# Optimization experiments

Hardware: AMD Instinct MI355X
Metric: run time of the kernel (lower is better)

Reference implementation:

```python
import jax, jax.numpy as jnp
import numpy as np
from jax import lax

T, D = 1024, 2048          # tokens, hidden
E, I = 32, 1408            # routed experts, expert intermediate
K = 6                      # top_k
N_GROUP, TOPK_GROUP = 8, 3
ROUTED_SCALE = 2.5
SHARED_I = 2 * I           # n_shared_experts * moe_intermediate_size


def setup_inputs() -> dict:
    key = jax.random.key(0)
    ks = jax.random.split(key, 9)
    s = lambda k, shape, fan: jax.random.normal(k, shape, jnp.float32) * (fan ** -0.5)
    return {
        "hidden_states": jax.random.normal(ks[0], (T, D), jnp.float32),
        "gate_w": s(ks[1], (D, E), D),
        "e_score_correction_bias": jax.random.normal(ks[2], (E,), jnp.float32) * 0.1,
        "w_gate": s(ks[3], (E, D, I), D),
        "w_up": s(ks[4], (E, D, I), D),
        "w_down": s(ks[5], (E, I, D), I),
        "ws_gate": s(ks[6], (D, SHARED_I), D),
        "ws_up": s(ks[7], (D, SHARED_I), D),
        "ws_down": s(ks[8], (SHARED_I, D), SHARED_I),
    }


def _route(x, gate_w, bias):
    """DeepSeek noaux_tc grouped top-k with sigmoid scoring."""
    logits = x @ gate_w                       # [T, E]
    scores = jax.nn.sigmoid(logits)
    scores_corr = scores + bias[None, :]
    # group scores = sum of top-2 corrected scores within each group
    g = scores_corr.reshape(-1, N_GROUP, E // N_GROUP)
    group_scores = lax.top_k(g, 2)[0].sum(-1)            # [T, n_group]
    _, gidx = lax.top_k(group_scores, TOPK_GROUP)        # [T, topk_group]
    gmask = jax.nn.one_hot(gidx, N_GROUP, dtype=scores.dtype).sum(1)  # [T, n_group]
    emask = jnp.repeat(gmask, E // N_GROUP, axis=-1)     # [T, E]
    masked = jnp.where(emask > 0, scores_corr, -jnp.inf)
    _, topk_idx = lax.top_k(masked, K)                   # [T, K]
    w = jnp.take_along_axis(scores, topk_idx, axis=-1)   # weights from UNcorrected scores
    w = w / (w.sum(-1, keepdims=True) + 1e-20)           # norm_topk_prob=True
    return topk_idx, w


def reference(hidden_states, gate_w, e_score_correction_bias,
              w_gate, w_up, w_down, ws_gate, ws_up, ws_down):
    x = hidden_states                                    # [T, D]
    topk_idx, topk_w = _route(x, gate_w, e_score_correction_bias)

    # combine weights as a sparse [T, E] matrix (K nonzeros per row)
    tok = jnp.arange(x.shape[0])[:, None]
    combine = jnp.zeros((x.shape[0], E), x.dtype).at[tok, topk_idx].add(topk_w)

    # routed experts: SwiGLU FFN per expert (dense-dispatch reference)
    h = jax.nn.silu(jnp.einsum('td,edi->eti', x, w_gate))
    h = h * jnp.einsum('td,edi->eti', x, w_up)           # [E, T, I]
    y = jnp.einsum('eti,eid->etd', h, w_down)            # [E, T, D]
    routed = jnp.einsum('te,etd->td', combine, y) * ROUTED_SCALE

    # shared experts MLP (SiluAndMul)
    shared = (jax.nn.silu(x @ ws_gate) * (x @ ws_up)) @ ws_down
    return routed + shared
```

## Files before the change

### kernel.cpp

```cpp
#include <hip/hip_runtime.h>

#define T_TOK 1024
#define D_HID 2048
#define NEXP 32
#define I_EXP 1408
#define TOPK 6
#define NGRP 8
#define GSIZE 4
#define TOPG 3
#define SHI 2816
#define RSCALE 2.5f

typedef __attribute__((ext_vector_type(8))) short short8;
typedef __attribute__((ext_vector_type(4))) float floatx4;

__device__ __forceinline__ unsigned short f2b(float f) {
  unsigned int u = __float_as_uint(f);
  u += 0x7fffu + ((u >> 16) & 1u);
  return (unsigned short)(u >> 16);
}

__device__ __forceinline__ void gld_lds16(const void* g, void* l) {
  __builtin_amdgcn_global_load_lds(
      (const __attribute__((address_space(1))) unsigned int*)g,
      (__attribute__((address_space(3))) unsigned int*)l, 16, 0, 0);
}

__device__ __forceinline__ uint4 pack8(const float* v) {
  uint4 o;
  o.x = (unsigned)f2b(v[0]) | ((unsigned)f2b(v[1]) << 16);
  o.y = (unsigned)f2b(v[2]) | ((unsigned)f2b(v[3]) << 16);
  o.z = (unsigned)f2b(v[4]) | ((unsigned)f2b(v[5]) << 16);
  o.w = (unsigned)f2b(v[6]) | ((unsigned)f2b(v[7]) << 16);
  return o;
}

__device__ __forceinline__ uint2 pack4(const float* v) {
  uint2 o;
  o.x = (unsigned)f2b(v[0]) | ((unsigned)f2b(v[1]) << 16);
  o.y = (unsigned)f2b(v[2]) | ((unsigned)f2b(v[3]) << 16);
  return o;
}

__global__ __launch_bounds__(64) void k_route(
    const float* __restrict__ x, const float* __restrict__ gw,
    const float* __restrict__ bias, int* __restrict__ tki, float* __restrict__ tkw)
{
  int t = blockIdx.x;
  __shared__ float xs[D_HID];
  __shared__ float sc[NEXP], cor[NEXP];
  int lane = threadIdx.x;
  for (int d = lane * 4; d < D_HID; d += 64 * 4)
    *(float4*)(xs + d) = *(const float4*)(x + (size_t)t * D_HID + d);
  __syncthreads();
  if (lane < NEXP) {
    float acc = 0.f;
    for (int d = 0; d < D_HID; ++d) acc += xs[d] * gw[d * NEXP + lane];
    float s = 1.f / (1.f + expf(-acc));
    sc[lane] = s;
    cor[lane] = s + bias[lane];
  }
  __syncthreads();
  if (lane == 0) {
    float gs[NGRP];
    for (int g = 0; g < NGRP; ++g) {
      float m1 = -INFINITY, m2 = -INFINITY;
      for (int j = 0; j < GSIZE; ++j) {
        float v = cor[g * GSIZE + j];
        if (v > m1) { m2 = m1; m1 = v; } else if (v > m2) m2 = v;
      }
      gs[g] = m1 + m2;
    }
    unsigned gmask = 0;
    for (int rr = 0; rr < TOPG; ++rr) {
      int bi = -1; float bv = -INFINITY;
      for (int g = 0; g < NGRP; ++g)
        if (!((gmask >> g) & 1) && gs[g] > bv) { bv = gs[g]; bi = g; }
      gmask |= 1u << bi;
    }
    unsigned used = 0;
    float wsum = 0.f;
    int idxs[TOPK]; float wsel[TOPK];
    for (int rr = 0; rr < TOPK; ++rr) {
      int bi = -1; float bv = -INFINITY;
      for (int e = 0; e < NEXP; ++e) {
        if (!((gmask >> (e / GSIZE)) & 1)) continue;
        if ((used >> e) & 1) continue;
        if (cor[e] > bv) { bv = cor[e]; bi = e; }
      }
      used |= 1u << bi;
      idxs[rr] = bi; wsel[rr] = sc[bi]; wsum += sc[bi];
    }
    float inv = 1.f / (wsum + 1e-20f);
    for (int rr = 0; rr < TOPK; ++rr) {
      tki[t * TOPK + rr] = idxs[rr];
      tkw[t * TOPK + rr] = wsel[rr] * inv;
    }
  }
}

__global__ __launch_bounds__(256) void k_count(const int* __restrict__ tki,
                                               int* __restrict__ cnt, int* __restrict__ offp)
{
  __shared__ int c[NEXP];
  if (threadIdx.x < NEXP) c[threadIdx.x] = 0;
  __syncthreads();
  for (int i = threadIdx.x; i < T_TOK * TOPK; i += 256) atomicAdd(&c[tki[i]], 1);
  __syncthreads();
  if (threadIdx.x == 0) {
    int s = 0;
    for (int e = 0; e < NEXP; ++e) { offp[e] = s; cnt[e] = c[e]; s += c[e]; }
    offp[NEXP] = s;
  }
}

__global__ __launch_bounds__(64) void k_compact(
    const int* __restrict__ tki, const float* __restrict__ tkw,
    const int* __restrict__ offp, int* __restrict__ tok, float* __restrict__ wts)
{
  int e = blockIdx.x, lane = threadIdx.x;
  int base = offp[e];
  for (int t0 = 0; t0 < T_TOK; t0 += 64) {
    int t = t0 + lane;
    int found = -1;
    for (int j = 0; j < TOPK; ++j)
      if (tki[t * TOPK + j] == e) found = j;
    unsigned long long m = __ballot(found >= 0);
    if (found >= 0) {
      int pos = base + __popcll(m & ((1ull << lane) - 1ull));
      tok[pos] = t;
      wts[pos] = tkw[t * TOPK + found];
    }
    base += __popcll(m);
  }
}

__global__ __launch_bounds__(256) void k_cast(const float* __restrict__ x,
                                              unsigned short* __restrict__ xb, int n4)
{
  int i = blockIdx.x * 256 + threadIdx.x;
  if (i < n4) {
    float4 v = ((const float4*)x)[i];
    ushort4 o;
    o.x = f2b(v.x); o.y = f2b(v.y); o.z = f2b(v.z); o.w = f2b(v.w);
    ((ushort4*)xb)[i] = o;
  }
}


template<int N, int K>
__device__ __forceinline__ void gemm_gu(
    const unsigned short* __restrict__ xb,
    const float* __restrict__ wgp, const float* __restrict__ wup,
    const int* __restrict__ tok, int rowbase, int nrows,
    unsigned short* __restrict__ hout, int n0,
    unsigned short* As , unsigned short* Bls )
{
  const int tid = threadIdx.x;
  const int wid = tid >> 6, lane = tid & 63;
  const int c = lane & 15, r = lane >> 4;
  const int wr = wid >> 1, wc = wid & 1;

  const int mat = wid >> 2;
  const int bko = wid & 3;
  const float* bsrc = (mat ? wup : wgp) + (size_t)(bko * 8) * N + n0 + lane;
  const int bwoff = lane * 36 + bko * 8 + mat * 2304;

  int aoff[4];
  #pragma unroll
  for (int mf = 0; mf < 4; ++mf)
    aoff[mf] = (r * 256 + wr * 64 + mf * 16 + c) * 8;
  int boff[2];
  #pragma unroll
  for (int nf = 0; nf < 2; ++nf)
    boff[nf] = (wc * 32 + nf * 16 + c) * 36 + r * 8;

  constexpr int NK = K / 32;

  for (int m0 = 0; m0 < nrows; m0 += 256) {
    const unsigned short* ga;
    {
      int rl = min(m0 + (tid & 255), nrows - 1);
      int tA = tok ? tok[rowbase + rl] : (rowbase + rl);
      ga = xb + (size_t)tA * K + (tid >> 8) * 8;
    }

    floatx4 accg[4][2] = {};
    floatx4 accu[4][2] = {};
    float br[8];

    #pragma unroll
    for (int j = 0; j < 8; ++j) br[j] = bsrc[(size_t)j * N];
    { uint4 pw = pack8(br); *(uint4*)&Bls[bwoff] = pw; }
    gld_lds16(ga, As + (size_t)tid * 8);
    gld_lds16(ga + 16, As + (size_t)(512 + tid) * 8);
    #pragma unroll
    for (int j = 0; j < 8; ++j) br[j] = bsrc[(size_t)(32 + j) * N];
    __syncthreads();

    int b = 0;
    for (int kt = 0; kt < NK; ++kt) {
      if (kt + 1 < NK) {
        { uint4 pw = pack8(br); *(uint4*)&Bls[(b ^ 1) * 4608 + bwoff] = pw; }
        const unsigned short* gap = ga + (kt + 1) * 32;
        gld_lds16(gap, As + (size_t)((b ^ 1) * 8192 + tid * 8));
        gld_lds16(gap + 16, As + (size_t)((b ^ 1) * 8192 + 4096 + tid * 8));
      }
      if (kt + 2 < NK) {
        const float* bs = bsrc + (size_t)(kt + 2) * 32 * N;
        #pragma unroll
        for (int j = 0; j < 8; ++j) br[j] = bs[(size_t)j * N];
      }
      short8 af[4];
      #pragma unroll
      for (int mf = 0; mf < 4; ++mf)
        af[mf] = *(const short8*)(As + b * 8192 + aoff[mf]);
      #pragma unroll
      for (int nf = 0; nf < 2; ++nf) {
        short8 fg = *(const short8*)(Bls + b * 4608 + boff[nf]);
        short8 fu = *(const short8*)(Bls + b * 4608 + 2304 + boff[nf]);
        #pragma unroll
        for (int mf = 0; mf < 4; ++mf) {
          accg[mf][nf] = __builtin_amdgcn_mfma_f32_16x16x32_bf16(af[mf], fg, accg[mf][nf], 0, 0, 0);
          accu[mf][nf] = __builtin_amdgcn_mfma_f32_16x16x32_bf16(af[mf], fu, accu[mf][nf], 0, 0, 0);
        }
      }
      __syncthreads();
      b ^= 1;
    }

    #pragma unroll
    for (int mf = 0; mf < 4; ++mf)
      #pragma unroll
      for (int nf = 0; nf < 2; ++nf)
        #pragma unroll
        for (int v = 0; v < 4; ++v) {
          int rr = wr * 64 + mf * 16 + r * 4 + v;
          if (m0 + rr < nrows) {
            float g = accg[mf][nf][v], u = accu[mf][nf][v];
            float s = g / (1.f + __expf(-g));
            hout[(size_t)(rowbase + m0 + rr) * N + n0 + wc * 32 + nf * 16 + c] = f2b(s * u);
          }
        }
  }
}

template<int N, int K>
__device__ __forceinline__ void gemm_dn(
    const unsigned short* __restrict__ hin,
    const float* __restrict__ wdp,
    const int* __restrict__ tok, const float* __restrict__ wts,
    int rowbase, int nrows,
    float* __restrict__ out, int n0,
    unsigned short* As , unsigned short* Bls )
{
  const int tid = threadIdx.x;
  const int wid = tid >> 6, lane = tid & 63;
  const int c = lane & 15, r = lane >> 4;
  const int wr = wid >> 1, wc = wid & 1;

  const int bko = wid & 3;
  const int half = wid >> 2;
  const float* bsrc = wdp + (size_t)(bko * 8 + half * 4) * N + n0 + lane;
  const int bwoff = lane * 36 + bko * 8 + half * 4;

  int aoff[4];
  #pragma unroll
  for (int mf = 0; mf < 4; ++mf)
    aoff[mf] = (r * 256 + wr * 64 + mf * 16 + c) * 8;
  int boff[2];
  #pragma unroll
  for (int nf = 0; nf < 2; ++nf)
    boff[nf] = (wc * 32 + nf * 16 + c) * 36 + r * 8;

  constexpr int NK = K / 32;

  for (int m0 = 0; m0 < nrows; m0 += 256) {
    const unsigned short* ga;
    {
      int rl = min(m0 + (tid & 255), nrows - 1);
      ga = hin + (size_t)(rowbase + rl) * K + (tid >> 8) * 8;
    }

    floatx4 acc[4][2] = {};
    float br[4];

    #pragma unroll
    for (int j = 0; j < 4; ++j) br[j] = bsrc[(size_t)j * N];
    { uint2 pw = pack4(br); *(uint2*)&Bls[bwoff] = pw; }
    gld_lds16(ga, As + (size_t)tid * 8);
    gld_lds16(ga + 16, As + (size_t)(512 + tid) * 8);
    #pragma unroll
    for (int j = 0; j < 4; ++j) br[j] = bsrc[(size_t)(32 + j) * N];
    __syncthreads();

    int b = 0;
    for (int kt = 0; kt < NK; ++kt) {
      if (kt + 1 < NK) {
        { uint2 pw = pack4(br); *(uint2*)&Bls[(b ^ 1) * 2304 + bwoff] = pw; }
        const unsigned short* gap = ga + (kt + 1) * 32;
        gld_lds16(gap, As + (size_t)((b ^ 1) * 8192 + tid * 8));
        gld_lds16(gap + 16, As + (size_t)((b ^ 1) * 8192 + 4096 + tid * 8));
      }
      if (kt + 2 < NK) {
        const float* bs = bsrc + (size_t)(kt + 2) * 32 * N;
        #pragma unroll
        for (int j = 0; j < 4; ++j) br[j] = bs[(size_t)j * N];
      }
      short8 af[4];
      #pragma unroll
      for (int mf = 0; mf < 4; ++mf)
        af[mf] = *(const short8*)(As + b * 8192 + aoff[mf]);
      #pragma unroll
      for (int nf = 0; nf < 2; ++nf) {
        short8 fd = *(const short8*)(Bls + b * 2304 + boff[nf]);
        #pragma unroll
        for (int mf = 0; mf < 4; ++mf)
          acc[mf][nf] = __builtin_amdgcn_mfma_f32_16x16x32_bf16(af[mf], fd, acc[mf][nf], 0, 0, 0);
      }
      __syncthreads();
      b ^= 1;
    }

    #pragma unroll
    for (int mf = 0; mf < 4; ++mf)
      #pragma unroll
      for (int nf = 0; nf < 2; ++nf)
        #pragma unroll
        for (int v = 0; v < 4; ++v) {
          int rr = wr * 64 + mf * 16 + r * 4 + v;
          if (m0 + rr < nrows) {
            int grow = rowbase + m0 + rr;
            int tk = tok ? tok[grow] : grow;
            float w = wts ? wts[grow] * RSCALE : 1.0f;
            atomicAdd(&out[(size_t)tk * N + n0 + wc * 32 + nf * 16 + c],
                      w * acc[mf][nf][v]);
          }
        }
  }
}

__global__ __launch_bounds__(512, 4) void k_gu6(
    const unsigned short* __restrict__ xb,
    const float* __restrict__ wg, const float* __restrict__ wu,
    const float* __restrict__ wsg, const float* __restrict__ wsu,
    const int* __restrict__ offp, const int* __restrict__ cnt,
    const int* __restrict__ tok,
    unsigned short* __restrict__ hb, unsigned short* __restrict__ sh)
{
  __shared__ __align__(16) unsigned short As[2][8192];
  __shared__ __align__(16) unsigned short Bls[2][2][2304];
  const int ey = blockIdx.y;
  const int n0 = blockIdx.x * 64;
  if (ey < NEXP) {
    if (n0 >= I_EXP) return;
    int rowbase = offp[ey], nrows = cnt[ey];
    if (nrows <= 0) return;
    gemm_gu<I_EXP, D_HID>(xb, wg + (size_t)ey * D_HID * I_EXP,
                          wu + (size_t)ey * D_HID * I_EXP,
                          tok, rowbase, nrows, hb, n0,
                          &As[0][0], &Bls[0][0][0]);
  } else {
    gemm_gu<SHI, D_HID>(xb, wsg, wsu, nullptr, (ey - NEXP) * 256, 256,
                        sh, n0, &As[0][0], &Bls[0][0][0]);
  }
}

__global__ __launch_bounds__(512, 4) void k_dn6(
    const unsigned short* __restrict__ hb, const unsigned short* __restrict__ sh,
    const float* __restrict__ wd, const float* __restrict__ wsd,
    const int* __restrict__ offp, const int* __restrict__ cnt,
    const int* __restrict__ tok, const float* __restrict__ wts,
    float* __restrict__ out)
{
  __shared__ __align__(16) unsigned short As[2][8192];
  __shared__ __align__(16) unsigned short Bls[2][2304];
  const int ey = blockIdx.y;
  const int n0 = blockIdx.x * 64;
  if (ey < NEXP) {
    int rowbase = offp[ey], nrows = cnt[ey];
    if (nrows <= 0) return;
    gemm_dn<D_HID, I_EXP>(hb, wd + (size_t)ey * I_EXP * D_HID,
                          tok, wts, rowbase, nrows, out, n0,
                          &As[0][0], &Bls[0][0]);
  } else {
    gemm_dn<D_HID, SHI>(sh, wsd, nullptr, nullptr, (ey - NEXP) * 256, 256,
                        out, n0, &As[0][0], &Bls[0][0]);
  }
}

extern "C" void kernel_launch(void* const* d_in, const int* in_sizes, int n_in,
                              void* d_out, int out_size, void* d_ws, size_t ws_size,
                              hipStream_t stream) {
  const float* x    = (const float*)d_in[0];
  const float* gw   = (const float*)d_in[1];
  const float* bias = (const float*)d_in[2];
  const float* wg   = (const float*)d_in[3];
  const float* wu   = (const float*)d_in[4];
  const float* wd   = (const float*)d_in[5];
  const float* wsg  = (const float*)d_in[6];
  const float* wsu  = (const float*)d_in[7];
  const float* wsd  = (const float*)d_in[8];
  float* out = (float*)d_out;

  char* ws = (char*)d_ws;
  size_t o = 0;
  auto take = [&](size_t bytes) {
    char* p = ws + o;
    o += (bytes + 255) & ~(size_t)255;
    return p;
  };
  int*   tki  = (int*)  take((size_t)T_TOK * TOPK * 4);
  float* tkw  = (float*)take((size_t)T_TOK * TOPK * 4);
  int*   cnt  = (int*)  take(NEXP * 4);
  int*   offp = (int*)  take((NEXP + 1) * 4);
  int*   tok  = (int*)  take((size_t)T_TOK * TOPK * 4);
  float* wts  = (float*)take((size_t)T_TOK * TOPK * 4);
  unsigned short* xb = (unsigned short*)take((size_t)T_TOK * D_HID * 2);
  unsigned short* hb = (unsigned short*)take((size_t)T_TOK * TOPK * I_EXP * 2);
  unsigned short* sh = (unsigned short*)take((size_t)T_TOK * SHI * 2);

  (void)hipMemsetAsync(out, 0, (size_t)T_TOK * D_HID * sizeof(float), stream);
  k_route<<<T_TOK, 64, 0, stream>>>(x, gw, bias, tki, tkw);
  k_count<<<1, 256, 0, stream>>>(tki, cnt, offp);
  k_compact<<<NEXP, 64, 0, stream>>>(tki, tkw, offp, tok, wts);
  k_cast<<<(T_TOK * D_HID / 4 + 255) / 256, 256, 0, stream>>>(x, xb, T_TOK * D_HID / 4);

  k_gu6<<<dim3(SHI / 64, NEXP + 4), 512, 0, stream>>>(
      xb, wg, wu, wsg, wsu, offp, cnt, tok, hb, sh);
  k_dn6<<<dim3(D_HID / 64, NEXP + 4), 512, 0, stream>>>(
      hb, sh, wd, wsd, offp, cnt, tok, wts, out);
}
```

Baseline: 1.025 ms.

## Drop LDS staging and split gate/up GEMMs into separate register-direct kernels

Replaces the LDS double-buffered GEMM with one where each wave loads its A fragments directly from global memory and converts fp32 B weights into registers itself, with no shared memory or barriers. The fused gate+up kernel becomes two launches: the gate GEMM writes bf16 intermediates and the up GEMM reads them back to apply SiLU-mul. Tiles shrink to 32 columns with 256-thread blocks to raise the block count and occupancy. In exchange, B weight tiles are no longer shared across waves, so there is more redundant global traffic, plus an extra intermediate buffer round trip and an extra launch.

New measurement: 1.377 ms. +34.4%, slower.

```diff
diff --git a/kernel.cpp b/kernel.cpp
--- a/kernel.cpp
+++ b/kernel.cpp
@@ -20,26 +20,17 @@
   return (unsigned short)(u >> 16);
 }
 
-__device__ __forceinline__ void gld_lds16(const void* g, void* l) {
-  __builtin_amdgcn_global_load_lds(
-      (const __attribute__((address_space(1))) unsigned int*)g,
-      (__attribute__((address_space(3))) unsigned int*)l, 16, 0, 0);
-}
-
-__device__ __forceinline__ uint4 pack8(const float* v) {
-  uint4 o;
-  o.x = (unsigned)f2b(v[0]) | ((unsigned)f2b(v[1]) << 16);
-  o.y = (unsigned)f2b(v[2]) | ((unsigned)f2b(v[3]) << 16);
-  o.z = (unsigned)f2b(v[4]) | ((unsigned)f2b(v[5]) << 16);
-  o.w = (unsigned)f2b(v[6]) | ((unsigned)f2b(v[7]) << 16);
-  return o;
-}
-
-__device__ __forceinline__ uint2 pack4(const float* v) {
-  uint2 o;
-  o.x = (unsigned)f2b(v[0]) | ((unsigned)f2b(v[1]) << 16);
-  o.y = (unsigned)f2b(v[2]) | ((unsigned)f2b(v[3]) << 16);
-  return o;
+__device__ __forceinline__ float b2f(unsigned short s) {
+  return __uint_as_float((unsigned)s << 16);
+}
+
+__device__ __forceinline__ short8 pack8s(const float* v) {
+  union { uint4 u; short8 s; } o;
+  o.u.x = (unsigned)f2b(v[0]) | ((unsigned)f2b(v[1]) << 16);
+  o.u.y = (unsigned)f2b(v[2]) | ((unsigned)f2b(v[3]) << 16);
+  o.u.z = (unsigned)f2b(v[4]) | ((unsigned)f2b(v[5]) << 16);
+  o.u.w = (unsigned)f2b(v[6]) | ((unsigned)f2b(v[7]) << 16);
+  return o.s;
 }
 
 __global__ __launch_bounds__(64) void k_route(
@@ -148,85 +139,48 @@
 }
 
 
-template<int N, int K>
-__device__ __forceinline__ void gemm_gu(
-    const unsigned short* __restrict__ xb,
-    const float* __restrict__ wgp, const float* __restrict__ wup,
+template<int KD, bool FUSE>
+__device__ __forceinline__ void gemm_pre(
+    const unsigned short* __restrict__ Ab,
     const int* __restrict__ tok, int rowbase, int nrows,
-    unsigned short* __restrict__ hout, int n0,
-    unsigned short* As , unsigned short* Bls )
+    const float* __restrict__ B, int N,
+    const unsigned short* __restrict__ Gp,
+    unsigned short* __restrict__ O, int n0)
 {
   const int tid = threadIdx.x;
-  const int wid = tid >> 6, lane = tid & 63;
+  const int w = tid >> 6, lane = tid & 63;
   const int c = lane & 15, r = lane >> 4;
-  const int wr = wid >> 1, wc = wid & 1;
-
-  const int mat = wid >> 2;
-  const int bko = wid & 3;
-  const float* bsrc = (mat ? wup : wgp) + (size_t)(bko * 8) * N + n0 + lane;
-  const int bwoff = lane * 36 + bko * 8 + mat * 2304;
-
-  int aoff[4];
-  #pragma unroll
-  for (int mf = 0; mf < 4; ++mf)
-    aoff[mf] = (r * 256 + wr * 64 + mf * 16 + c) * 8;
-  int boff[2];
-  #pragma unroll
-  for (int nf = 0; nf < 2; ++nf)
-    boff[nf] = (wc * 32 + nf * 16 + c) * 36 + r * 8;
-
-  constexpr int NK = K / 32;
+  const float* bp0 = B + (size_t)(r * 8) * N + n0 + c;
+  const float* bp1 = bp0 + 16;
 
   for (int m0 = 0; m0 < nrows; m0 += 256) {
-    const unsigned short* ga;
-    {
-      int rl = min(m0 + (tid & 255), nrows - 1);
-      int tA = tok ? tok[rowbase + rl] : (rowbase + rl);
-      ga = xb + (size_t)tA * K + (tid >> 8) * 8;
-    }
-
-    floatx4 accg[4][2] = {};
-    floatx4 accu[4][2] = {};
-    float br[8];
-
+    const unsigned short* ap[4];
     #pragma unroll
-    for (int j = 0; j < 8; ++j) br[j] = bsrc[(size_t)j * N];
-    { uint4 pw = pack8(br); *(uint4*)&Bls[bwoff] = pw; }
-    gld_lds16(ga, As + (size_t)tid * 8);
-    gld_lds16(ga + 16, As + (size_t)(512 + tid) * 8);
-    #pragma unroll
-    for (int j = 0; j < 8; ++j) br[j] = bsrc[(size_t)(32 + j) * N];
-    __syncthreads();
-
-    int b = 0;
-    for (int kt = 0; kt < NK; ++kt) {
-      if (kt + 1 < NK) {
-        { uint4 pw = pack8(br); *(uint4*)&Bls[(b ^ 1) * 4608 + bwoff] = pw; }
-        const unsigned short* gap = ga + (kt + 1) * 32;
-        gld_lds16(gap, As + (size_t)((b ^ 1) * 8192 + tid * 8));
-        gld_lds16(gap + 16, As + (size_t)((b ^ 1) * 8192 + 4096 + tid * 8));
+    for (int mf = 0; mf < 4; ++mf) {
+      int rl = min(m0 + w * 64 + mf * 16 + c, nrows - 1);
+      int ta = tok ? tok[rowbase + rl] : (rowbase + rl);
+      ap[mf] = Ab + (size_t)ta * KD + r * 8;
+    }
+
+    floatx4 acc[4][2] = {};
+
+    #pragma unroll 1
+    for (int kt = 0; kt < KD / 32; ++kt) {
+      float b0[8], b1[8];
+      #pragma unroll
+      for (int j = 0; j < 8; ++j) b0[j] = bp0[(size_t)(kt * 32 + j) * N];
+      #pragma unroll
+      for (int j = 0; j < 8; ++j) b1[j] = bp1[(size_t)(kt * 32 + j) * N];
+      short8 af[4];
+      #pragma unroll
+      for (int mf = 0; mf < 4; ++mf)
+        af[mf] = *(const short8*)(ap[mf] + kt * 32);
+      short8 f0 = pack8s(b0), f1 = pack8s(b1);
+      #pragma unroll
+      for (int mf = 0; mf < 4; ++mf) {
+        acc[mf][0] = __builtin_amdgcn_mfma_f32_16x16x32_bf16(af[mf], f0, acc[mf][0], 0, 0, 0);
+        acc[mf][1] = __builtin_amdgcn_mfma_f32_16x16x32_bf16(af[mf], f1, acc[mf][1], 0, 0, 0);
       }
-      if (kt + 2 < NK) {
-        const float* bs = bsrc + (size_t)(kt + 2) * 32 * N;
-        #pragma unroll
-        for (int j = 0; j < 8; ++j) br[j] = bs[(size_t)j * N];
-      }
-      short8 af[4];
-      #pragma unroll
-      for (int mf = 0; mf < 4; ++mf)
-        af[mf] = *(const short8*)(As + b * 8192 + aoff[mf]);
-      #pragma unroll
-      for (int nf = 0; nf < 2; ++nf) {
-        short8 fg = *(const short8*)(Bls + b * 4608 + boff[nf]);
-        short8 fu = *(const short8*)(Bls + b * 4608 + 2304 + boff[nf]);
-        #pragma unroll
-        for (int mf = 0; mf < 4; ++mf) {
-          accg[mf][nf] = __builtin_amdgcn_mfma_f32_16x16x32_bf16(af[mf], fg, accg[mf][nf], 0, 0, 0);
-          accu[mf][nf] = __builtin_amdgcn_mfma_f32_16x16x32_bf16(af[mf], fu, accu[mf][nf], 0, 0, 0);
-        }
-      }
-      __syncthreads();
-      b ^= 1;
     }
 
     #pragma unroll
@@ -235,91 +189,63 @@
       for (int nf = 0; nf < 2; ++nf)
         #pragma unroll
         for (int v = 0; v < 4; ++v) {
-          int rr = wr * 64 + mf * 16 + r * 4 + v;
+          int rr = w * 64 + mf * 16 + r * 4 + v;
           if (m0 + rr < nrows) {
-            float g = accg[mf][nf][v], u = accu[mf][nf][v];
-            float s = g / (1.f + __expf(-g));
-            hout[(size_t)(rowbase + m0 + rr) * N + n0 + wc * 32 + nf * 16 + c] = f2b(s * u);
+            size_t oi = (size_t)(rowbase + m0 + rr) * N + n0 + nf * 16 + c;
+            float a = acc[mf][nf][v];
+            if (FUSE) {
+              float g = b2f(Gp[oi]);
+              float s = g / (1.f + __expf(-g));
+              O[oi] = f2b(s * a);
+            } else {
+              O[oi] = f2b(a);
+            }
           }
         }
   }
 }
 
-template<int N, int K>
-__device__ __forceinline__ void gemm_dn(
-    const unsigned short* __restrict__ hin,
-    const float* __restrict__ wdp,
-    const int* __restrict__ tok, const float* __restrict__ wts,
+template<int KD>
+__device__ __forceinline__ void gemm_dn2(
+    const unsigned short* __restrict__ Ab,
     int rowbase, int nrows,
-    float* __restrict__ out, int n0,
-    unsigned short* As , unsigned short* Bls )
+    const float* __restrict__ B, int N,
+    const int* __restrict__ tok, const float* __restrict__ wts, float scale,
+    float* __restrict__ out, int n0)
 {
   const int tid = threadIdx.x;
-  const int wid = tid >> 6, lane = tid & 63;
+  const int w = tid >> 6, lane = tid & 63;
   const int c = lane & 15, r = lane >> 4;
-  const int wr = wid >> 1, wc = wid & 1;
-
-  const int bko = wid & 3;
-  const int half = wid >> 2;
-  const float* bsrc = wdp + (size_t)(bko * 8 + half * 4) * N + n0 + lane;
-  const int bwoff = lane * 36 + bko * 8 + half * 4;
-
-  int aoff[4];
-  #pragma unroll
-  for (int mf = 0; mf < 4; ++mf)
-    aoff[mf] = (r * 256 + wr * 64 + mf * 16 + c) * 8;
-  int boff[2];
-  #pragma unroll
-  for (int nf = 0; nf < 2; ++nf)
-    boff[nf] = (wc * 32 + nf * 16 + c) * 36 + r * 8;
-
-  constexpr int NK = K / 32;
+  const float* bp0 = B + (size_t)(r * 8) * N + n0 + c;
+  const float* bp1 = bp0 + 16;
 
   for (int m0 = 0; m0 < nrows; m0 += 256) {
-    const unsigned short* ga;
-    {
-      int rl = min(m0 + (tid & 255), nrows - 1);
-      ga = hin + (size_t)(rowbase + rl) * K + (tid >> 8) * 8;
+    const unsigned short* ap[4];
+    #pragma unroll
+    for (int mf = 0; mf < 4; ++mf) {
+      int rl = min(m0 + w * 64 + mf * 16 + c, nrows - 1);
+      ap[mf] = Ab + (size_t)(rowbase + rl) * KD + r * 8;
     }
 
     floatx4 acc[4][2] = {};
-    float br[4];
-
-    #pragma unroll
-    for (int j = 0; j < 4; ++j) br[j] = bsrc[(size_t)j * N];
-    { uint2 pw = pack4(br); *(uint2*)&Bls[bwoff] = pw; }
-    gld_lds16(ga, As + (size_t)tid * 8);
-    gld_lds16(ga + 16, As + (size_t)(512 + tid) * 8);
-    #pragma unroll
-    for (int j = 0; j < 4; ++j) br[j] = bsrc[(size_t)(32 + j) * N];
-    __syncthreads();
-
-    int b = 0;
-    for (int kt = 0; kt < NK; ++kt) {
-      if (kt + 1 < NK) {
-        { uint2 pw = pack4(br); *(uint2*)&Bls[(b ^ 1) * 2304 + bwoff] = pw; }
-        const unsigned short* gap = ga + (kt + 1) * 32;
-        gld_lds16(gap, As + (size_t)((b ^ 1) * 8192 + tid * 8));
-        gld_lds16(gap + 16, As + (size_t)((b ^ 1) * 8192 + 4096 + tid * 8));
+
+    #pragma unroll 1
+    for (int kt = 0; kt < KD / 32; ++kt) {
+      float b0[8], b1[8];
+      #pragma unroll
+      for (int j = 0; j < 8; ++j) b0[j] = bp0[(size_t)(kt * 32 + j) * N];
+      #pragma unroll
+      for (int j = 0; j < 8; ++j) b1[j] = bp1[(size_t)(kt * 32 + j) * N];
+      short8 af[4];
+      #pragma unroll
+      for (int mf = 0; mf < 4; ++mf)
+        af[mf] = *(const short8*)(ap[mf] + kt * 32);
+      short8 f0 = pack8s(b0), f1 = pack8s(b1);
+      #pragma unroll
+      for (int mf = 0; mf < 4; ++mf) {
+        acc[mf][0] = __builtin_amdgcn_mfma_f32_16x16x32_bf16(af[mf], f0, acc[mf][0], 0, 0, 0);
+        acc[mf][1] = __builtin_amdgcn_mfma_f32_16x16x32_bf16(af[mf], f1, acc[mf][1], 0, 0, 0);
       }
-      if (kt + 2 < NK) {
-        const float* bs = bsrc + (size_t)(kt + 2) * 32 * N;
-        #pragma unroll
-        for (int j = 0; j < 4; ++j) br[j] = bs[(size_t)j * N];
-      }
-      short8 af[4];
-      #pragma unroll
-      for (int mf = 0; mf < 4; ++mf)
-        af[mf] = *(const short8*)(As + b * 8192 + aoff[mf]);
-      #pragma unroll
-      for (int nf = 0; nf < 2; ++nf) {
-        short8 fd = *(const short8*)(Bls + b * 2304 + boff[nf]);
-        #pragma unroll
-        for (int mf = 0; mf < 4; ++mf)
-          acc[mf][nf] = __builtin_amdgcn_mfma_f32_16x16x32_bf16(af[mf], fd, acc[mf][nf], 0, 0, 0);
-      }
-      __syncthreads();
-      b ^= 1;
     }
 
     #pragma unroll
@@ -328,64 +254,74 @@
       for (int nf = 0; nf < 2; ++nf)
         #pragma unroll
         for (int v = 0; v < 4; ++v) {
-          int rr = wr * 64 + mf * 16 + r * 4 + v;
+          int rr = w * 64 + mf * 16 + r * 4 + v;
           if (m0 + rr < nrows) {
             int grow = rowbase + m0 + rr;
             int tk = tok ? tok[grow] : grow;
-            float w = wts ? wts[grow] * RSCALE : 1.0f;
-            atomicAdd(&out[(size_t)tk * N + n0 + wc * 32 + nf * 16 + c],
-                      w * acc[mf][nf][v]);
+            float wgt = wts ? wts[grow] * scale : scale;
+            atomicAdd(&out[(size_t)tk * N + n0 + nf * 16 + c], wgt * acc[mf][nf][v]);
           }
         }
   }
 }
 
-__global__ __launch_bounds__(512, 4) void k_gu6(
+__global__ __launch_bounds__(256, 4) void k_gate(
     const unsigned short* __restrict__ xb,
-    const float* __restrict__ wg, const float* __restrict__ wu,
-    const float* __restrict__ wsg, const float* __restrict__ wsu,
+    const float* __restrict__ wg, const float* __restrict__ wsg,
     const int* __restrict__ offp, const int* __restrict__ cnt,
     const int* __restrict__ tok,
-    unsigned short* __restrict__ hb, unsigned short* __restrict__ sh)
-{
-  __shared__ __align__(16) unsigned short As[2][8192];
-  __shared__ __align__(16) unsigned short Bls[2][2][2304];
-  const int ey = blockIdx.y;
-  const int n0 = blockIdx.x * 64;
+    unsigned short* __restrict__ gR, unsigned short* __restrict__ gS)
+{
+  const int ey = blockIdx.y, n0 = blockIdx.x * 32;
   if (ey < NEXP) {
     if (n0 >= I_EXP) return;
-    int rowbase = offp[ey], nrows = cnt[ey];
-    if (nrows <= 0) return;
-    gemm_gu<I_EXP, D_HID>(xb, wg + (size_t)ey * D_HID * I_EXP,
-                          wu + (size_t)ey * D_HID * I_EXP,
-                          tok, rowbase, nrows, hb, n0,
-                          &As[0][0], &Bls[0][0][0]);
+    int rb = offp[ey], nr = cnt[ey];
+    if (nr <= 0) return;
+    gemm_pre<D_HID, false>(xb, tok, rb, nr, wg + (size_t)ey * D_HID * I_EXP,
+                           I_EXP, nullptr, gR, n0);
   } else {
-    gemm_gu<SHI, D_HID>(xb, wsg, wsu, nullptr, (ey - NEXP) * 256, 256,
-                        sh, n0, &As[0][0], &Bls[0][0][0]);
-  }
-}
-
-__global__ __launch_bounds__(512, 4) void k_dn6(
-    const unsigned short* __restrict__ hb, const unsigned short* __restrict__ sh,
+    gemm_pre<D_HID, false>(xb, nullptr, (ey - NEXP) * 256, 256, wsg, SHI,
+                           nullptr, gS, n0);
+  }
+}
+
+__global__ __launch_bounds__(256, 4) void k_up(
+    const unsigned short* __restrict__ xb,
+    const float* __restrict__ wu, const float* __restrict__ wsu,
+    const int* __restrict__ offp, const int* __restrict__ cnt,
+    const int* __restrict__ tok,
+    const unsigned short* __restrict__ gR, const unsigned short* __restrict__ gS,
+    unsigned short* __restrict__ hR, unsigned short* __restrict__ hS)
+{
+  const int ey = blockIdx.y, n0 = blockIdx.x * 32;
+  if (ey < NEXP) {
+    if (n0 >= I_EXP) return;
+    int rb = offp[ey], nr = cnt[ey];
+    if (nr <= 0) return;
+    gemm_pre<D_HID, true>(xb, tok, rb, nr, wu + (size_t)ey * D_HID * I_EXP,
+                          I_EXP, gR, hR, n0);
+  } else {
+    gemm_pre<D_HID, true>(xb, nullptr, (ey - NEXP) * 256, 256, wsu, SHI,
+                          gS, hS, n0);
+  }
+}
+
+__global__ __launch_bounds__(256, 4) void k_down7(
+    const unsigned short* __restrict__ hR, const unsigned short* __restrict__ hS,
     const float* __restrict__ wd, const float* __restrict__ wsd,
     const int* __restrict__ offp, const int* __restrict__ cnt,
     const int* __restrict__ tok, const float* __restrict__ wts,
     float* __restrict__ out)
 {
-  __shared__ __align__(16) unsigned short As[2][8192];
-  __shared__ __align__(16) unsigned short Bls[2][2304];
-  const int ey = blockIdx.y;
-  const int n0 = blockIdx.x * 64;
+  const int ey = blockIdx.y, n0 = blockIdx.x * 32;
   if (ey < NEXP) {
-    int rowbase = offp[ey], nrows = cnt[ey];
-    if (nrows <= 0) return;
-    gemm_dn<D_HID, I_EXP>(hb, wd + (size_t)ey * I_EXP * D_HID,
-                          tok, wts, rowbase, nrows, out, n0,
-                          &As[0][0], &Bls[0][0]);
+    int rb = offp[ey], nr = cnt[ey];
+    if (nr <= 0) return;
+    gemm_dn2<I_EXP>(hR, rb, nr, wd + (size_t)ey * I_EXP * D_HID, D_HID,
+                    tok, wts, RSCALE, out, n0);
   } else {
-    gemm_dn<D_HID, SHI>(sh, wsd, nullptr, nullptr, (ey - NEXP) * 256, 256,
-                        out, n0, &As[0][0], &Bls[0][0]);
+    gemm_dn2<SHI>(hS, (ey - NEXP) * 256, 256, wsd, D_HID,
+                  nullptr, nullptr, 1.0f, out, n0);
   }
 }
 
@@ -417,8 +353,10 @@
   int*   tok  = (int*)  take((size_t)T_TOK * TOPK * 4);
   float* wts  = (float*)take((size_t)T_TOK * TOPK * 4);
   unsigned short* xb = (unsigned short*)take((size_t)T_TOK * D_HID * 2);
-  unsigned short* hb = (unsigned short*)take((size_t)T_TOK * TOPK * I_EXP * 2);
-  unsigned short* sh = (unsigned short*)take((size_t)T_TOK * SHI * 2);
+  unsigned short* gR = (unsigned short*)take((size_t)T_TOK * TOPK * I_EXP * 2);
+  unsigned short* gS = (unsigned short*)take((size_t)T_TOK * SHI * 2);
+  unsigned short* hR = (unsigned short*)take((size_t)T_TOK * TOPK * I_EXP * 2);
+  unsigned short* hS = (unsigned short*)take((size_t)T_TOK * SHI * 2);
 
   (void)hipMemsetAsync(out, 0, (size_t)T_TOK * D_HID * sizeof(float), stream);
   k_route<<<T_TOK, 64, 0, stream>>>(x, gw, bias, tki, tkw);
@@ -426,8 +364,10 @@
   k_compact<<<NEXP, 64, 0, stream>>>(tki, tkw, offp, tok, wts);
   k_cast<<<(T_TOK * D_HID / 4 + 255) / 256, 256, 0, stream>>>(x, xb, T_TOK * D_HID / 4);
 
-  k_gu6<<<dim3(SHI / 64, NEXP + 4), 512, 0, stream>>>(
-      xb, wg, wu, wsg, wsu, offp, cnt, tok, hb, sh);
-  k_dn6<<<dim3(D_HID / 64, NEXP + 4), 512, 0, stream>>>(
-      hb, sh, wd, wsd, offp, cnt, tok, wts, out);
-}
+  k_gate<<<dim3(SHI / 32, NEXP + 4), 256, 0, stream>>>(
+      xb, wg, wsg, offp, cnt, tok, gR, gS);
+  k_up<<<dim3(SHI / 32, NEXP + 4), 256, 0, stream>>>(
+      xb, wu, wsu, offp, cnt, tok, gR, gS, hR, hS);
+  k_down7<<<dim3(D_HID / 32, NEXP + 4), 256, 0, stream>>>(
+      hR, hS, wd, wsd, offp, cnt, tok, wts, out);
+}
```

## Pre-gather tokens into tile-packed bf16 layout and flatten expert GEMM grids

Applied to the files above, without the earlier changes.

Replaces the plain bf16 cast with a prep kernel that gathers each expert's routed tokens, pads them to 256-row chunks, and stores the activations in the exact LDS tile layout, so the GEMMs stream contiguous 16-byte chunks instead of indirect per-token rows. The gate/up kernel now writes its hidden output in the same tiled layout for the down kernel. Both GEMM kernels use a flat 1D grid with no idle blocks, where the old 2D grid wasted blocks on column tiles past the expert width. The cost is an extra gather pass that writes about 56 MB of padded activations, plus more workspace.

New measurement: 1.004 ms. -2.0%, faster.

```diff
diff --git a/kernel.cpp b/kernel.cpp
--- a/kernel.cpp
+++ b/kernel.cpp
@@ -100,7 +100,8 @@
 }
 
 __global__ __launch_bounds__(256) void k_count(const int* __restrict__ tki,
-                                               int* __restrict__ cnt, int* __restrict__ offp)
+                                               int* __restrict__ cnt, int* __restrict__ offp,
+                                               int* __restrict__ poff)
 {
   __shared__ int c[NEXP];
   if (threadIdx.x < NEXP) c[threadIdx.x] = 0;
@@ -108,9 +109,13 @@
   for (int i = threadIdx.x; i < T_TOK * TOPK; i += 256) atomicAdd(&c[tki[i]], 1);
   __syncthreads();
   if (threadIdx.x == 0) {
-    int s = 0;
-    for (int e = 0; e < NEXP; ++e) { offp[e] = s; cnt[e] = c[e]; s += c[e]; }
-    offp[NEXP] = s;
+    int s = 0, p = 0;
+    for (int e = 0; e < NEXP; ++e) {
+      offp[e] = s; cnt[e] = c[e]; poff[e] = p;
+      s += c[e];
+      p += 256 * ((c[e] + 255) / 256);
+    }
+    offp[NEXP] = s; poff[NEXP] = p;
   }
 }
 
@@ -135,26 +140,58 @@
   }
 }
 
-__global__ __launch_bounds__(256) void k_cast(const float* __restrict__ x,
-                                              unsigned short* __restrict__ xb, int n4)
-{
-  int i = blockIdx.x * 256 + threadIdx.x;
-  if (i < n4) {
-    float4 v = ((const float4*)x)[i];
-    ushort4 o;
-    o.x = f2b(v.x); o.y = f2b(v.y); o.z = f2b(v.z); o.w = f2b(v.w);
-    ((ushort4*)xb)[i] = o;
-  }
-}
-
-
-template<int N, int K>
-__device__ __forceinline__ void gemm_gu(
-    const unsigned short* __restrict__ xb,
+__global__ __launch_bounds__(256) void k_prep(
+    const float* __restrict__ x,
+    const int* __restrict__ offp, const int* __restrict__ cnt,
+    const int* __restrict__ poff, const int* __restrict__ tok,
+    unsigned short* __restrict__ Ap, unsigned short* __restrict__ ApS)
+{
+  const int ey = blockIdx.x, ch = blockIdx.y, m = threadIdx.x;
+  const int* tk = nullptr;
+  int nr;
+  unsigned short* dst;
+  if (ey < NEXP) {
+    nr = cnt[ey];
+    int pad = poff[ey + 1] - poff[ey];
+    if (ch * 256 >= pad) return;
+    dst = Ap + ((size_t)(poff[ey] >> 8) + ch) * 64 * 8192;
+    tk = tok + offp[ey];
+  } else {
+    nr = T_TOK;
+    dst = ApS + (size_t)ch * 64 * 8192;
+  }
+  int grow = ch * 256 + m;
+  const float* src = nullptr;
+  if (grow < nr) {
+    int t = tk ? tk[grow] : grow;
+    src = x + (size_t)t * D_HID;
+  }
+  for (int kt = 0; kt < 64; ++kt) {
+    #pragma unroll
+    for (int ko = 0; ko < 4; ++ko) {
+      uint4 w = {0u, 0u, 0u, 0u};
+      if (src) {
+        const float* s = src + kt * 32 + ko * 8;
+        float4 a = *(const float4*)s;
+        float4 b = *(const float4*)(s + 4);
+        w.x = (unsigned)f2b(a.x) | ((unsigned)f2b(a.y) << 16);
+        w.y = (unsigned)f2b(a.z) | ((unsigned)f2b(a.w) << 16);
+        w.z = (unsigned)f2b(b.x) | ((unsigned)f2b(b.y) << 16);
+        w.w = (unsigned)f2b(b.z) | ((unsigned)f2b(b.w) << 16);
+      }
+      *(uint4*)(dst + (size_t)kt * 8192 + (ko * 256 + m) * 8) = w;
+    }
+  }
+}
+
+
+template<int N, int NKT_H>
+__device__ __forceinline__ void gu_body(
+    const unsigned short* __restrict__ Abase,
     const float* __restrict__ wgp, const float* __restrict__ wup,
-    const int* __restrict__ tok, int rowbase, int nrows,
-    unsigned short* __restrict__ hout, int n0,
-    unsigned short* As , unsigned short* Bls )
+    unsigned short* __restrict__ hbase,
+    int c0, int c1, int nrows, int n0,
+    unsigned short* As, unsigned short* Bls)
 {
   const int tid = threadIdx.x;
   const int wid = tid >> 6, lane = tid & 63;
@@ -175,15 +212,8 @@
   for (int nf = 0; nf < 2; ++nf)
     boff[nf] = (wc * 32 + nf * 16 + c) * 36 + r * 8;
 
-  constexpr int NK = K / 32;
-
-  for (int m0 = 0; m0 < nrows; m0 += 256) {
-    const unsigned short* ga;
-    {
-      int rl = min(m0 + (tid & 255), nrows - 1);
-      int tA = tok ? tok[rowbase + rl] : (rowbase + rl);
-      ga = xb + (size_t)tA * K + (tid >> 8) * 8;
-    }
+  for (int ch = c0; ch < c1; ++ch) {
+    const unsigned short* Ach = Abase + (size_t)ch * 64 * 8192;
 
     floatx4 accg[4][2] = {};
     floatx4 accu[4][2] = {};
@@ -192,21 +222,21 @@
     #pragma unroll
     for (int j = 0; j < 8; ++j) br[j] = bsrc[(size_t)j * N];
     { uint4 pw = pack8(br); *(uint4*)&Bls[bwoff] = pw; }
-    gld_lds16(ga, As + (size_t)tid * 8);
-    gld_lds16(ga + 16, As + (size_t)(512 + tid) * 8);
+    gld_lds16(Ach + tid * 8, As + tid * 8);
+    gld_lds16(Ach + (512 + tid) * 8, As + (512 + tid) * 8);
     #pragma unroll
     for (int j = 0; j < 8; ++j) br[j] = bsrc[(size_t)(32 + j) * N];
     __syncthreads();
 
     int b = 0;
-    for (int kt = 0; kt < NK; ++kt) {
-      if (kt + 1 < NK) {
+    for (int kt = 0; kt < 64; ++kt) {
+      if (kt + 1 < 64) {
         { uint4 pw = pack8(br); *(uint4*)&Bls[(b ^ 1) * 4608 + bwoff] = pw; }
-        const unsigned short* gap = ga + (kt + 1) * 32;
-        gld_lds16(gap, As + (size_t)((b ^ 1) * 8192 + tid * 8));
-        gld_lds16(gap + 16, As + (size_t)((b ^ 1) * 8192 + 4096 + tid * 8));
-      }
-      if (kt + 2 < NK) {
+        const unsigned short* Ak = Ach + (size_t)(kt + 1) * 8192;
+        gld_lds16(Ak + tid * 8, As + (b ^ 1) * 8192 + tid * 8);
+        gld_lds16(Ak + (512 + tid) * 8, As + (b ^ 1) * 8192 + (512 + tid) * 8);
+      }
+      if (kt + 2 < 64) {
         const float* bs = bsrc + (size_t)(kt + 2) * 32 * N;
         #pragma unroll
         for (int j = 0; j < 8; ++j) br[j] = bs[(size_t)j * N];
@@ -229,30 +259,34 @@
       b ^= 1;
     }
 
+    unsigned short* hch = hbase + (size_t)ch * NKT_H * 8192;
+    int m0 = ch * 256;
     #pragma unroll
     for (int mf = 0; mf < 4; ++mf)
       #pragma unroll
       for (int nf = 0; nf < 2; ++nf)
         #pragma unroll
         for (int v = 0; v < 4; ++v) {
-          int rr = wr * 64 + mf * 16 + r * 4 + v;
-          if (m0 + rr < nrows) {
+          int mrow = wr * 64 + mf * 16 + r * 4 + v;
+          if (m0 + mrow < nrows) {
+            int col = n0 + wc * 32 + nf * 16 + c;
             float g = accg[mf][nf][v], u = accu[mf][nf][v];
             float s = g / (1.f + __expf(-g));
-            hout[(size_t)(rowbase + m0 + rr) * N + n0 + wc * 32 + nf * 16 + c] = f2b(s * u);
+            hch[(size_t)(col >> 5) * 8192 + (((col >> 3) & 3) * 256 + mrow) * 8 + (col & 7)] =
+                f2b(s * u);
           }
         }
   }
 }
 
-template<int N, int K>
-__device__ __forceinline__ void gemm_dn(
-    const unsigned short* __restrict__ hin,
+template<int NKT>
+__device__ __forceinline__ void dn_body(
+    const unsigned short* __restrict__ Abase,
     const float* __restrict__ wdp,
-    const int* __restrict__ tok, const float* __restrict__ wts,
-    int rowbase, int nrows,
-    float* __restrict__ out, int n0,
-    unsigned short* As , unsigned short* Bls )
+    const int* __restrict__ tokp, const float* __restrict__ wtsp, float scale,
+    float* __restrict__ out,
+    int c0, int c1, int nrows, int n0,
+    unsigned short* As, unsigned short* Bls)
 {
   const int tid = threadIdx.x;
   const int wid = tid >> 6, lane = tid & 63;
@@ -261,7 +295,7 @@
 
   const int bko = wid & 3;
   const int half = wid >> 2;
-  const float* bsrc = wdp + (size_t)(bko * 8 + half * 4) * N + n0 + lane;
+  const float* bsrc = wdp + (size_t)(bko * 8 + half * 4) * D_HID + n0 + lane;
   const int bwoff = lane * 36 + bko * 8 + half * 4;
 
   int aoff[4];
@@ -273,39 +307,33 @@
   for (int nf = 0; nf < 2; ++nf)
     boff[nf] = (wc * 32 + nf * 16 + c) * 36 + r * 8;
 
-  constexpr int NK = K / 32;
-
-  for (int m0 = 0; m0 < nrows; m0 += 256) {
-    const unsigned short* ga;
-    {
-      int rl = min(m0 + (tid & 255), nrows - 1);
-      ga = hin + (size_t)(rowbase + rl) * K + (tid >> 8) * 8;
-    }
+  for (int ch = c0; ch < c1; ++ch) {
+    const unsigned short* Ach = Abase + (size_t)ch * NKT * 8192;
 
     floatx4 acc[4][2] = {};
     float br[4];
 
     #pragma unroll
-    for (int j = 0; j < 4; ++j) br[j] = bsrc[(size_t)j * N];
+    for (int j = 0; j < 4; ++j) br[j] = bsrc[(size_t)j * D_HID];
     { uint2 pw = pack4(br); *(uint2*)&Bls[bwoff] = pw; }
-    gld_lds16(ga, As + (size_t)tid * 8);
-    gld_lds16(ga + 16, As + (size_t)(512 + tid) * 8);
-    #pragma unroll
-    for (int j = 0; j < 4; ++j) br[j] = bsrc[(size_t)(32 + j) * N];
+    gld_lds16(Ach + tid * 8, As + tid * 8);
+    gld_lds16(Ach + (512 + tid) * 8, As + (512 + tid) * 8);
+    #pragma unroll
+    for (int j = 0; j < 4; ++j) br[j] = bsrc[(size_t)(32 + j) * D_HID];
     __syncthreads();
 
     int b = 0;
-    for (int kt = 0; kt < NK; ++kt) {
-      if (kt + 1 < NK) {
+    for (int kt = 0; kt < NKT; ++kt) {
+      if (kt + 1 < NKT) {
         { uint2 pw = pack4(br); *(uint2*)&Bls[(b ^ 1) * 2304 + bwoff] = pw; }
-        const unsigned short* gap = ga + (kt + 1) * 32;
-        gld_lds16(gap, As + (size_t)((b ^ 1) * 8192 + tid * 8));
-        gld_lds16(gap + 16, As + (size_t)((b ^ 1) * 8192 + 4096 + tid * 8));
-      }
-      if (kt + 2 < NK) {
-        const float* bs = bsrc + (size_t)(kt + 2) * 32 * N;
-        #pragma unroll
-        for (int j = 0; j < 4; ++j) br[j] = bs[(size_t)j * N];
+        const unsigned short* Ak = Ach + (size_t)(kt + 1) * 8192;
+        gld_lds16(Ak + tid * 8, As + (b ^ 1) * 8192 + tid * 8);
+        gld_lds16(Ak + (512 + tid) * 8, As + (b ^ 1) * 8192 + (512 + tid) * 8);
+      }
+      if (kt + 2 < NKT) {
+        const float* bs = bsrc + (size_t)(kt + 2) * 32 * D_HID;
+        #pragma unroll
+        for (int j = 0; j < 4; ++j) br[j] = bs[(size_t)j * D_HID];
       }
       short8 af[4];
       #pragma unroll
@@ -322,70 +350,76 @@
       b ^= 1;
     }
 
+    int m0 = ch * 256;
     #pragma unroll
     for (int mf = 0; mf < 4; ++mf)
       #pragma unroll
       for (int nf = 0; nf < 2; ++nf)
         #pragma unroll
         for (int v = 0; v < 4; ++v) {
-          int rr = wr * 64 + mf * 16 + r * 4 + v;
-          if (m0 + rr < nrows) {
-            int grow = rowbase + m0 + rr;
-            int tk = tok ? tok[grow] : grow;
-            float w = wts ? wts[grow] * RSCALE : 1.0f;
-            atomicAdd(&out[(size_t)tk * N + n0 + wc * 32 + nf * 16 + c],
+          int mrow = wr * 64 + mf * 16 + r * 4 + v;
+          if (m0 + mrow < nrows) {
+            int grow = m0 + mrow;
+            int tk = tokp ? tokp[grow] : grow;
+            float w = wtsp ? wtsp[grow] * scale : scale;
+            atomicAdd(&out[(size_t)tk * D_HID + n0 + wc * 32 + nf * 16 + c],
                       w * acc[mf][nf][v]);
           }
         }
   }
 }
 
-__global__ __launch_bounds__(512, 4) void k_gu6(
-    const unsigned short* __restrict__ xb,
+__global__ __launch_bounds__(512, 4) void k_gu9(
+    const unsigned short* __restrict__ Ap, const unsigned short* __restrict__ ApS,
     const float* __restrict__ wg, const float* __restrict__ wu,
     const float* __restrict__ wsg, const float* __restrict__ wsu,
-    const int* __restrict__ offp, const int* __restrict__ cnt,
-    const int* __restrict__ tok,
-    unsigned short* __restrict__ hb, unsigned short* __restrict__ sh)
-{
-  __shared__ __align__(16) unsigned short As[2][8192];
-  __shared__ __align__(16) unsigned short Bls[2][2][2304];
-  const int ey = blockIdx.y;
-  const int n0 = blockIdx.x * 64;
-  if (ey < NEXP) {
-    if (n0 >= I_EXP) return;
-    int rowbase = offp[ey], nrows = cnt[ey];
-    if (nrows <= 0) return;
-    gemm_gu<I_EXP, D_HID>(xb, wg + (size_t)ey * D_HID * I_EXP,
-                          wu + (size_t)ey * D_HID * I_EXP,
-                          tok, rowbase, nrows, hb, n0,
-                          &As[0][0], &Bls[0][0][0]);
+    const int* __restrict__ cnt, const int* __restrict__ poff,
+    unsigned short* __restrict__ hR, unsigned short* __restrict__ hS)
+{
+  __shared__ __align__(16) unsigned short As[2 * 8192];
+  __shared__ __align__(16) unsigned short Bls[2 * 4608];
+  int bid = blockIdx.x;
+  if (bid < 176) {
+    int x = bid % 44, ch = bid / 44;
+    gu_body<SHI, 88>(ApS, wsg, wsu, hS, ch, ch + 1, T_TOK, x * 64, As, Bls);
   } else {
-    gemm_gu<SHI, D_HID>(xb, wsg, wsu, nullptr, (ey - NEXP) * 256, 256,
-                        sh, n0, &As[0][0], &Bls[0][0][0]);
-  }
-}
-
-__global__ __launch_bounds__(512, 4) void k_dn6(
-    const unsigned short* __restrict__ hb, const unsigned short* __restrict__ sh,
+    int rel = bid - 176;
+    int e = rel / 22, x = rel % 22;
+    int nr = cnt[e];
+    if (nr <= 0) return;
+    int cb = poff[e] >> 8;
+    gu_body<I_EXP, 44>(Ap + (size_t)cb * 64 * 8192,
+                       wg + (size_t)e * D_HID * I_EXP,
+                       wu + (size_t)e * D_HID * I_EXP,
+                       hR + (size_t)cb * 44 * 8192,
+                       0, (nr + 255) >> 8, nr, x * 64, As, Bls);
+  }
+}
+
+__global__ __launch_bounds__(512, 4) void k_dn9(
+    const unsigned short* __restrict__ hR, const unsigned short* __restrict__ hS,
     const float* __restrict__ wd, const float* __restrict__ wsd,
     const int* __restrict__ offp, const int* __restrict__ cnt,
+    const int* __restrict__ poff,
     const int* __restrict__ tok, const float* __restrict__ wts,
     float* __restrict__ out)
 {
-  __shared__ __align__(16) unsigned short As[2][8192];
-  __shared__ __align__(16) unsigned short Bls[2][2304];
-  const int ey = blockIdx.y;
-  const int n0 = blockIdx.x * 64;
-  if (ey < NEXP) {
-    int rowbase = offp[ey], nrows = cnt[ey];
-    if (nrows <= 0) return;
-    gemm_dn<D_HID, I_EXP>(hb, wd + (size_t)ey * I_EXP * D_HID,
-                          tok, wts, rowbase, nrows, out, n0,
-                          &As[0][0], &Bls[0][0]);
+  __shared__ __align__(16) unsigned short As[2 * 8192];
+  __shared__ __align__(16) unsigned short Bls[2 * 2304];
+  int bid = blockIdx.x;
+  if (bid < 128) {
+    int x = bid & 31, ch = bid >> 5;
+    dn_body<88>(hS, wsd, nullptr, nullptr, 1.0f, out, ch, ch + 1, T_TOK, x * 64, As, Bls);
   } else {
-    gemm_dn<D_HID, SHI>(sh, wsd, nullptr, nullptr, (ey - NEXP) * 256, 256,
-                        out, n0, &As[0][0], &Bls[0][0]);
+    int rel = bid - 128;
+    int e = rel >> 5, x = rel & 31;
+    int nr = cnt[e];
+    if (nr <= 0) return;
+    int cb = poff[e] >> 8;
+    dn_body<44>(hR + (size_t)cb * 44 * 8192,
+                wd + (size_t)e * I_EXP * D_HID,
+                tok + offp[e], wts + offp[e], RSCALE,
+                out, 0, (nr + 255) >> 8, nr, x * 64, As, Bls);
   }
 }
 
@@ -414,20 +448,22 @@
   float* tkw  = (float*)take((size_t)T_TOK * TOPK * 4);
   int*   cnt  = (int*)  take(NEXP * 4);
   int*   offp = (int*)  take((NEXP + 1) * 4);
+  int*   poff = (int*)  take((NEXP + 1) * 4);
   int*   tok  = (int*)  take((size_t)T_TOK * TOPK * 4);
   float* wts  = (float*)take((size_t)T_TOK * TOPK * 4);
-  unsigned short* xb = (unsigned short*)take((size_t)T_TOK * D_HID * 2);
-  unsigned short* hb = (unsigned short*)take((size_t)T_TOK * TOPK * I_EXP * 2);
-  unsigned short* sh = (unsigned short*)take((size_t)T_TOK * SHI * 2);
+  unsigned short* Ap  = (unsigned short*)take((size_t)14336 * D_HID * 2);
+  unsigned short* ApS = (unsigned short*)take((size_t)4 * 64 * 8192 * 2);
+  unsigned short* hR  = (unsigned short*)take((size_t)56 * 44 * 8192 * 2);
+  unsigned short* hS  = (unsigned short*)take((size_t)4 * 88 * 8192 * 2);
 
   (void)hipMemsetAsync(out, 0, (size_t)T_TOK * D_HID * sizeof(float), stream);
   k_route<<<T_TOK, 64, 0, stream>>>(x, gw, bias, tki, tkw);
-  k_count<<<1, 256, 0, stream>>>(tki, cnt, offp);
+  k_count<<<1, 256, 0, stream>>>(tki, cnt, offp, poff);
   k_compact<<<NEXP, 64, 0, stream>>>(tki, tkw, offp, tok, wts);
-  k_cast<<<(T_TOK * D_HID / 4 + 255) / 256, 256, 0, stream>>>(x, xb, T_TOK * D_HID / 4);
-
-  k_gu6<<<dim3(SHI / 64, NEXP + 4), 512, 0, stream>>>(
-      xb, wg, wu, wsg, wsu, offp, cnt, tok, hb, sh);
-  k_dn6<<<dim3(D_HID / 64, NEXP + 4), 512, 0, stream>>>(
-      hb, sh, wd, wsd, offp, cnt, tok, wts, out);
-}
+  k_prep<<<dim3(NEXP + 1, 4), 256, 0, stream>>>(x, offp, cnt, poff, tok, Ap, ApS);
+
+  k_gu9<<<176 + 22 * NEXP, 512, 0, stream>>>(
+      Ap, ApS, wg, wu, wsg, wsu, cnt, poff, hR, hS);
+  k_dn9<<<128 + 32 * NEXP, 512, 0, stream>>>(
+      hR, hS, wd, wsd, offp, cnt, poff, tok, wts, out);
+}
```
